# Kernel tuning notes

Measured on AMD Instinct MI355X. Metric: run time of the kernel, lower is better.

Reference implementation:

```python
import jax, jax.numpy as jnp
import numpy as np

IN_DIM = 4096
OUT_DIM = 4096
RANK = 16
BATCH = 4
SEQ = 2048


def setup_inputs() -> dict:
    key = jax.random.key(0)
    ks = jax.random.split(key, 7)
    x = jax.random.normal(ks[0], (BATCH, SEQ, IN_DIM), dtype=jnp.float32)
    org_weight = jax.random.normal(ks[1], (OUT_DIM, IN_DIM), dtype=jnp.float32) * 0.02
    org_bias = jax.random.normal(ks[2], (OUT_DIM,), dtype=jnp.float32) * 0.02
    hada_w1_a = jax.random.normal(ks[3], (OUT_DIM, RANK), dtype=jnp.float32) * 0.1
    hada_w1_b = jax.random.normal(ks[4], (RANK, IN_DIM), dtype=jnp.float32)
    hada_w2_a = jax.random.normal(ks[5], (OUT_DIM, RANK), dtype=jnp.float32) * 0.1
    hada_w2_b = jax.random.normal(ks[6], (RANK, IN_DIM), dtype=jnp.float32)
    scalar = jnp.ones((), dtype=jnp.float32)
    return {
        "x": x,
        "org_weight": org_weight,
        "org_bias": org_bias,
        "hada_w1_a": hada_w1_a,
        "hada_w1_b": hada_w1_b,
        "hada_w2_a": hada_w2_a,
        "hada_w2_b": hada_w2_b,
        "scalar": scalar,
    }


def reference(x, org_weight, org_bias, hada_w1_a, hada_w1_b, hada_w2_a, hada_w2_b, scalar):
    scale = jnp.asarray(1.0, dtype=hada_w1_b.dtype)   # self.scale = 1.0
    multiplier = jnp.asarray(1.0, dtype=x.dtype)       # self.multiplier = 1.0
    # base = F.linear(x, org_weight, org_bias)
    base = jnp.einsum("bsi,oi->bso", x, org_weight) + org_bias
    # diff_weight = (w1a @ w1b) * (w2a @ w2b) * scale * scalar  -> [out, in]
    diff_weight = (hada_w1_a @ hada_w1_b) * (hada_w2_a @ hada_w2_b) * scale * scalar
    # delta = F.linear(x, diff_weight * multiplier)
    delta = jnp.einsum("bsi,oi->bso", x, diff_weight * multiplier)
    return base + delta
```

## Files before the change

kernel.cpp:

```cpp
#include <hip/hip_runtime.h>

#define IN_DIM 4096
#define OUT_DIM 4096
#define RANK 16
#define MDIM 8192

typedef unsigned short ushort_t;
typedef __attribute__((ext_vector_type(8))) short short8;
typedef __attribute__((ext_vector_type(4))) float floatx4;
typedef __attribute__((ext_vector_type(4))) ushort_t ushort4_t;
typedef __attribute__((ext_vector_type(2))) ushort_t ushort2_t;

__device__ __forceinline__ ushort_t f2b(float f) {
    union { float f; unsigned int i; } v; v.f = f;
    unsigned int u = v.i;
    u += 0x7FFFu + ((u >> 16) & 1u);
    return (ushort_t)(u >> 16);
}

#define GLOAD_LDS16(gp, lp)                                                    \
    __builtin_amdgcn_global_load_lds(                                          \
        (__attribute__((address_space(1))) void*)(gp),                         \
        (__attribute__((address_space(3))) void*)(lp), 16, 0, 0)

__global__ __launch_bounds__(256) void convx_kernel(
    const float4* __restrict__ x, ushort4_t* __restrict__ xb, int n4)
{
    int i = blockIdx.x * blockDim.x + threadIdx.x;
    int stride = gridDim.x * blockDim.x;
    for (; i < n4; i += stride) {
        float4 v = x[i];
        ushort4_t o;
        o.x = f2b(v.x); o.y = f2b(v.y); o.z = f2b(v.z); o.w = f2b(v.w);
        xb[i] = o;
    }
}

__global__ __launch_bounds__(256) void weff_kernel(
    const float* __restrict__ orgw,
    const float* __restrict__ w1a, const float* __restrict__ w1b,
    const float* __restrict__ w2a, const float* __restrict__ w2b,
    const float* __restrict__ scalar,
    ushort_t* __restrict__ weff)
{
    __shared__ float s1a[64 * RANK];
    __shared__ float s2a[64 * RANK];

    const int t  = threadIdx.x;
    const int i0 = blockIdx.x * 512 + t * 2;
    const int o0 = blockIdx.y * 64;

    for (int e = t; e < 64 * RANK; e += 256) {
        s1a[e] = w1a[o0 * RANK + e];
        s2a[e] = w2a[o0 * RANK + e];
    }

    float b1[RANK][2], b2[RANK][2];
    #pragma unroll
    for (int r = 0; r < RANK; ++r) {
        const float2 v1 = *(const float2*)&w1b[r * IN_DIM + i0];
        const float2 v2 = *(const float2*)&w2b[r * IN_DIM + i0];
        b1[r][0] = v1.x; b1[r][1] = v1.y;
        b2[r][0] = v2.x; b2[r][1] = v2.y;
    }
    __syncthreads();

    const float sc = scalar[0];
    for (int o = 0; o < 64; ++o) {
        float4 a1v[4], a2v[4];
        #pragma unroll
        for (int j = 0; j < 4; ++j) {
            a1v[j] = *(const float4*)&s1a[o * RANK + j * 4];
            a2v[j] = *(const float4*)&s2a[o * RANK + j * 4];
        }
        float p1_0 = 0.f, p1_1 = 0.f, p2_0 = 0.f, p2_1 = 0.f;
        #pragma unroll
        for (int j = 0; j < 4; ++j) {
            #pragma unroll
            for (int k = 0; k < 4; ++k) {
                const int r = j * 4 + k;
                const float a1 = (k == 0) ? a1v[j].x : (k == 1) ? a1v[j].y
                               : (k == 2) ? a1v[j].z : a1v[j].w;
                const float a2 = (k == 0) ? a2v[j].x : (k == 1) ? a2v[j].y
                               : (k == 2) ? a2v[j].z : a2v[j].w;
                p1_0 += a1 * b1[r][0]; p1_1 += a1 * b1[r][1];
                p2_0 += a2 * b2[r][0]; p2_1 += a2 * b2[r][1];
            }
        }
        const size_t idx = (size_t)(o0 + o) * IN_DIM + i0;
        const float2 ov = *(const float2*)&orgw[idx];
        ushort2_t st;
        st.x = f2b(ov.x + p1_0 * p2_0 * sc);
        st.y = f2b(ov.y + p1_1 * p2_1 * sc);
        *(ushort2_t*)&weff[idx] = st;
    }
}

#define BM 256
#define BN 256
#define BK 64

#define STAGE_A(buf, half, kcol)                                               \
    do {                                                                       \
        GLOAD_LDS16(gX0 + (size_t)(half) * (128 * IN_DIM) + (kcol),            \
                    (short*)&lA[buf][half][0][0] + w * 512);                   \
        GLOAD_LDS16(gX1 + (size_t)(half) * (128 * IN_DIM) + (kcol),            \
                    (short*)&lA[buf][half][0][0] + 4096 + w * 512);            \
    } while (0)

#define STAGE_B(buf, half, kcol)                                               \
    do {                                                                       \
        GLOAD_LDS16(gW0 + (size_t)(half) * (128 * IN_DIM) + (kcol),            \
                    (short*)&lB[buf][half][0][0] + w * 512);                   \
        GLOAD_LDS16(gW1 + (size_t)(half) * (128 * IN_DIM) + (kcol),            \
                    (short*)&lB[buf][half][0][0] + 4096 + w * 512);            \
    } while (0)

#define MFMA_(d, a, b) (d) = __builtin_amdgcn_mfma_f32_16x16x32_bf16((a), (b), (d), 0, 0, 0)

#define HALF_ITER(aB, bB, S1, S2, S3, S4)                                      \
    do {                                                                       \
        short8 a_lo[4][2], a_hi[4][2], b_lo[2][2], b_hi[2][2];                 \
        S1;                                                                    \
                           \
        _Pragma("unroll")                                                      \
        for (int mi = 0; mi < 4; ++mi) {                                       \
            a_lo[mi][0] = *(const short8*)((aB) + mi * 1024 + ok0);            \
            a_lo[mi][1] = *(const short8*)((aB) + mi * 1024 + ok1);            \
        }                                                                      \
        _Pragma("unroll")                                                      \
        for (int ni = 0; ni < 2; ++ni) {                                       \
            b_lo[ni][0] = *(const short8*)((bB) + ni * 1024 + ok0);            \
            b_lo[ni][1] = *(const short8*)((bB) + ni * 1024 + ok1);            \
        }                                                                      \
        asm volatile("" ::: "memory");                  \
                                     \
        _Pragma("unroll")                                                      \
        for (int mi = 0; mi < 4; ++mi) {                                       \
            a_hi[mi][0] = *(const short8*)((aB) + 4096 + mi * 1024 + ok0);     \
            a_hi[mi][1] = *(const short8*)((aB) + 4096 + mi * 1024 + ok1);     \
        }                                                                      \
        asm volatile("" ::: "memory");                  \
                                     \
        _Pragma("unroll")                                                      \
        for (int ni = 0; ni < 2; ++ni) {                                       \
            b_hi[ni][0] = *(const short8*)((bB) + 2048 + ni * 1024 + ok0);     \
            b_hi[ni][1] = *(const short8*)((bB) + 2048 + ni * 1024 + ok1);     \
        }                                                                      \
          \
        __builtin_amdgcn_s_barrier();                                          \
        asm volatile("s_waitcnt lgkmcnt(12)" ::: "memory");                    \
        __builtin_amdgcn_sched_barrier(0);                                     \
        __builtin_amdgcn_s_setprio(1);                                         \
        _Pragma("unroll")                                                      \
        for (int mi = 0; mi < 4; ++mi)                                         \
            _Pragma("unroll")                                                  \
            for (int ni = 0; ni < 2; ++ni) {                                   \
                MFMA_(acc[mi][ni], a_lo[mi][0], b_lo[ni][0]);                  \
                MFMA_(acc[mi][ni], a_lo[mi][1], b_lo[ni][1]);                  \
            }                                                                  \
        __builtin_amdgcn_s_setprio(0);                                         \
        __builtin_amdgcn_s_barrier();                                          \
                         \
        S2;                                                                    \
        __builtin_amdgcn_s_barrier();                                          \
        asm volatile("s_waitcnt lgkmcnt(4)" ::: "memory");                     \
        __builtin_amdgcn_sched_barrier(0);                                     \
        __builtin_amdgcn_s_setprio(1);                                         \
        _Pragma("unroll")                                                      \
        for (int mi = 0; mi < 4; ++mi)                                         \
            _Pragma("unroll")                                                  \
            for (int ni = 0; ni < 2; ++ni) {                                   \
                MFMA_(acc[4 + mi][ni], a_hi[mi][0], b_lo[ni][0]);              \
                MFMA_(acc[4 + mi][ni], a_hi[mi][1], b_lo[ni][1]);              \
            }                                                                  \
        __builtin_amdgcn_s_setprio(0);                                         \
        __builtin_amdgcn_s_barrier();                                          \
                                     \
        S3;                                                                    \
        __builtin_amdgcn_s_barrier();                                          \
        asm volatile("s_waitcnt lgkmcnt(0)" ::: "memory");                     \
        __builtin_amdgcn_sched_barrier(0);                                     \
        __builtin_amdgcn_s_setprio(1);                                         \
        _Pragma("unroll")                                                      \
        for (int mi = 0; mi < 4; ++mi)                                         \
            _Pragma("unroll")                                                  \
            for (int ni = 0; ni < 2; ++ni) {                                   \
                MFMA_(acc[4 + mi][2 + ni], a_hi[mi][0], b_hi[ni][0]);          \
                MFMA_(acc[4 + mi][2 + ni], a_hi[mi][1], b_hi[ni][1]);          \
            }                                                                  \
        __builtin_amdgcn_s_setprio(0);                                         \
        __builtin_amdgcn_s_barrier();                                          \
                  \
        S4;                                                                    \
        __builtin_amdgcn_s_barrier();                                          \
        __builtin_amdgcn_s_setprio(1);                                         \
        _Pragma("unroll")                                                      \
        for (int mi = 0; mi < 4; ++mi)                                         \
            _Pragma("unroll")                                                  \
            for (int ni = 0; ni < 2; ++ni) {                                   \
                MFMA_(acc[mi][2 + ni], a_lo[mi][0], b_hi[ni][0]);              \
                MFMA_(acc[mi][2 + ni], a_lo[mi][1], b_hi[ni][1]);              \
            }                                                                  \
        __builtin_amdgcn_s_setprio(0);                                         \
        asm volatile("s_waitcnt vmcnt(4)" ::: "memory");                       \
        __builtin_amdgcn_s_barrier();                                          \
    } while (0)

__global__ __launch_bounds__(512, 2) void gemm_kernel(
    const ushort_t* __restrict__ X,
    const ushort_t* __restrict__ W,
    const float* __restrict__ bias,
    float* __restrict__ out)
{
    __shared__ __align__(16) short lA[2][2][128][64];
    __shared__ __align__(16) short lB[2][2][128][64];

    const int t    = threadIdx.x;
    const int w    = t >> 6;
    const int lane = t & 63;
    const int quad = lane >> 4;
    const int r16  = lane & 15;
    const int wm   = w >> 2;
    const int wn   = w & 3;

    const int bid = blockIdx.y * gridDim.x + blockIdx.x;
    const int swz = (bid & 7) * 64 + (bid >> 3);
    const int m0  = (swz >> 4) * BM;
    const int n0  = (swz & 15) * BN;

    const int s0  = w * 64 + lane;
    const int s1  = 512 + s0;
    const int r0  = s0 >> 3, r1 = s1 >> 3;
    const int k80 = (s0 & 7) ^ (r0 & 7);
    const int k81 = (s1 & 7) ^ (r1 & 7);
    const ushort_t* gX0 = X + (size_t)(m0 + r0) * IN_DIM + k80 * 8;
    const ushort_t* gX1 = X + (size_t)(m0 + r1) * IN_DIM + k81 * 8;
    const ushort_t* gW0 = W + (size_t)(n0 + r0) * IN_DIM + k80 * 8;
    const ushort_t* gW1 = W + (size_t)(n0 + r1) * IN_DIM + k81 * 8;

    const short* aB0 = &lA[0][wm][r16][0];
    const short* aB1 = &lA[1][wm][r16][0];
    const short* bB0 = &lB[0][wn >> 1][(wn & 1) * 64 + r16][0];
    const short* bB1 = &lB[1][wn >> 1][(wn & 1) * 64 + r16][0];
    const int ok0 = ((0 + quad) ^ (r16 & 7)) << 3;
    const int ok1 = ((4 + quad) ^ (r16 & 7)) << 3;

    floatx4 acc[8][4];
    #pragma unroll
    for (int i = 0; i < 8; ++i)
        #pragma unroll
        for (int j = 0; j < 4; ++j)
            acc[i][j] = (floatx4){0.f, 0.f, 0.f, 0.f};

    STAGE_A(0, 0, 0);
    STAGE_A(0, 1, 0);
    STAGE_B(0, 0, 0);
    STAGE_B(0, 1, 0);
    STAGE_A(1, 0, 64);
    STAGE_A(1, 1, 64);
    asm volatile("s_waitcnt vmcnt(4)" ::: "memory");
    __builtin_amdgcn_s_barrier();

    for (int it = 0; it < IN_DIM / 128; ++it) {
        const int kmax = IN_DIM - 64;
        int kB1 = it * 128 + 64;  if (kB1 > kmax) kB1 = kmax;
        int kA2 = it * 128 + 128; if (kA2 > kmax) kA2 = kmax;
        int kA3 = it * 128 + 192; if (kA3 > kmax) kA3 = kmax;

        HALF_ITER(aB0, bB0,
                  STAGE_B(1, 0, kB1), STAGE_B(1, 1, kB1),
                  STAGE_A(0, 0, kA2), STAGE_A(0, 1, kA2));
        HALF_ITER(aB1, bB1,
                  STAGE_B(0, 0, kA2), STAGE_B(0, 1, kA2),
                  STAGE_A(1, 0, kA3), STAGE_A(1, 1, kA3));
    }

    #pragma unroll
    for (int ni = 0; ni < 4; ++ni) {
        const int gn = n0 + wn * 64 + ni * 16 + r16;
        const float bv = bias[gn];
        #pragma unroll
        for (int mi = 0; mi < 8; ++mi) {
            const int gm = m0 + wm * 128 + mi * 16 + quad * 4;
            #pragma unroll
            for (int rr = 0; rr < 4; ++rr)
                out[(size_t)(gm + rr) * OUT_DIM + gn] = acc[mi][ni][rr] + bv;
        }
    }
}

extern "C" void kernel_launch(void* const* d_in, const int* in_sizes, int n_in,
                              void* d_out, int out_size, void* d_ws, size_t ws_size,
                              hipStream_t stream) {
    const float* x      = (const float*)d_in[0];
    const float* orgw   = (const float*)d_in[1];
    const float* bias   = (const float*)d_in[2];
    const float* w1a    = (const float*)d_in[3];
    const float* w1b    = (const float*)d_in[4];
    const float* w2a    = (const float*)d_in[5];
    const float* w2b    = (const float*)d_in[6];
    const float* scalar = (const float*)d_in[7];

    ushort_t* xb   = (ushort_t*)d_ws;
    ushort_t* weff = (ushort_t*)d_ws + (size_t)MDIM * IN_DIM;
    float* out = (float*)d_out;

    const int n4 = MDIM * IN_DIM / 4;
    convx_kernel<<<2048, 256, 0, stream>>>((const float4*)x, (ushort4_t*)xb, n4);
    weff_kernel<<<dim3(IN_DIM / 512, OUT_DIM / 64), 256, 0, stream>>>(
        orgw, w1a, w1b, w2a, w2b, scalar, weff);
    gemm_kernel<<<dim3(OUT_DIM / BN, MDIM / BM), 512, 0, stream>>>(
        xb, weff, bias, out);
}
```

Baseline: 630.0 us.

## Merge x-conversion and weight-prep kernels and reorder GEMM LDS reads

Fuses the bf16 conversion of x and the effective-weight construction into one prep kernel, using a block-index split, so one launch replaces two and the two jobs can overlap. The weight loop is unrolled by 2 and loads the original weight before the rank-16 products. In the GEMM half-iteration, the LDS reads of the a_hi and b_hi fragments now sit between the MFMA phases instead of all being issued up front, and the waits become full lgkmcnt(0) waits without sched_barriers. This lowers register pressure and interleaves LDS traffic with staging, but it may expose more LDS latency.

Measured after the change: 556.7 us. -11.6%, faster.

```diff
diff --git a/kernel.cpp b/kernel.cpp
--- a/kernel.cpp
+++ b/kernel.cpp
@@ -23,20 +23,8 @@
         (__attribute__((address_space(1))) void*)(gp),                         \
         (__attribute__((address_space(3))) void*)(lp), 16, 0, 0)
 
-__global__ __launch_bounds__(256) void convx_kernel(
-    const float4* __restrict__ x, ushort4_t* __restrict__ xb, int n4)
-{
-    int i = blockIdx.x * blockDim.x + threadIdx.x;
-    int stride = gridDim.x * blockDim.x;
-    for (; i < n4; i += stride) {
-        float4 v = x[i];
-        ushort4_t o;
-        o.x = f2b(v.x); o.y = f2b(v.y); o.z = f2b(v.z); o.w = f2b(v.w);
-        xb[i] = o;
-    }
-}
-
-__global__ __launch_bounds__(256) void weff_kernel(
+__global__ __launch_bounds__(256) void prep_kernel(
+    const float4* __restrict__ x, ushort4_t* __restrict__ xb, int n4,
     const float* __restrict__ orgw,
     const float* __restrict__ w1a, const float* __restrict__ w1b,
     const float* __restrict__ w2a, const float* __restrict__ w2b,
@@ -46,53 +34,68 @@
     __shared__ float s1a[64 * RANK];
     __shared__ float s2a[64 * RANK];
 
-    const int t  = threadIdx.x;
-    const int i0 = blockIdx.x * 512 + t * 2;
-    const int o0 = blockIdx.y * 64;
-
-    for (int e = t; e < 64 * RANK; e += 256) {
-        s1a[e] = w1a[o0 * RANK + e];
-        s2a[e] = w2a[o0 * RANK + e];
-    }
-
-    float b1[RANK][2], b2[RANK][2];
-    #pragma unroll
-    for (int r = 0; r < RANK; ++r) {
-        const float2 v1 = *(const float2*)&w1b[r * IN_DIM + i0];
-        const float2 v2 = *(const float2*)&w2b[r * IN_DIM + i0];
-        b1[r][0] = v1.x; b1[r][1] = v1.y;
-        b2[r][0] = v2.x; b2[r][1] = v2.y;
-    }
-    __syncthreads();
-
-    const float sc = scalar[0];
-    for (int o = 0; o < 64; ++o) {
-        float4 a1v[4], a2v[4];
+    const int bid = blockIdx.x;
+    const int t   = threadIdx.x;
+
+    if (bid < 512) {
+        const int i0 = (bid & 7) * 512 + t * 2;
+        const int o0 = (bid >> 3) * 64;
+
+        for (int e = t; e < 64 * RANK; e += 256) {
+            s1a[e] = w1a[o0 * RANK + e];
+            s2a[e] = w2a[o0 * RANK + e];
+        }
+
+        float b1[RANK][2], b2[RANK][2];
         #pragma unroll
-        for (int j = 0; j < 4; ++j) {
-            a1v[j] = *(const float4*)&s1a[o * RANK + j * 4];
-            a2v[j] = *(const float4*)&s2a[o * RANK + j * 4];
-        }
-        float p1_0 = 0.f, p1_1 = 0.f, p2_0 = 0.f, p2_1 = 0.f;
-        #pragma unroll
-        for (int j = 0; j < 4; ++j) {
+        for (int r = 0; r < RANK; ++r) {
+            const float2 v1 = *(const float2*)&w1b[r * IN_DIM + i0];
+            const float2 v2 = *(const float2*)&w2b[r * IN_DIM + i0];
+            b1[r][0] = v1.x; b1[r][1] = v1.y;
+            b2[r][0] = v2.x; b2[r][1] = v2.y;
+        }
+        __syncthreads();
+
+        const float sc = scalar[0];
+        #pragma unroll 2
+        for (int o = 0; o < 64; ++o) {
+            const size_t idx = (size_t)(o0 + o) * IN_DIM + i0;
+            const float2 ov = *(const float2*)&orgw[idx];
+            float4 a1v[4], a2v[4];
             #pragma unroll
-            for (int k = 0; k < 4; ++k) {
-                const int r = j * 4 + k;
-                const float a1 = (k == 0) ? a1v[j].x : (k == 1) ? a1v[j].y
-                               : (k == 2) ? a1v[j].z : a1v[j].w;
-                const float a2 = (k == 0) ? a2v[j].x : (k == 1) ? a2v[j].y
-                               : (k == 2) ? a2v[j].z : a2v[j].w;
-                p1_0 += a1 * b1[r][0]; p1_1 += a1 * b1[r][1];
-                p2_0 += a2 * b2[r][0]; p2_1 += a2 * b2[r][1];
+            for (int j = 0; j < 4; ++j) {
+                a1v[j] = *(const float4*)&s1a[o * RANK + j * 4];
+                a2v[j] = *(const float4*)&s2a[o * RANK + j * 4];
             }
-        }
-        const size_t idx = (size_t)(o0 + o) * IN_DIM + i0;
-        const float2 ov = *(const float2*)&orgw[idx];
-        ushort2_t st;
-        st.x = f2b(ov.x + p1_0 * p2_0 * sc);
-        st.y = f2b(ov.y + p1_1 * p2_1 * sc);
-        *(ushort2_t*)&weff[idx] = st;
+            float p1_0 = 0.f, p1_1 = 0.f, p2_0 = 0.f, p2_1 = 0.f;
+            #pragma unroll
+            for (int j = 0; j < 4; ++j) {
+                #pragma unroll
+                for (int k = 0; k < 4; ++k) {
+                    const int r = j * 4 + k;
+                    const float a1 = (k == 0) ? a1v[j].x : (k == 1) ? a1v[j].y
+                                   : (k == 2) ? a1v[j].z : a1v[j].w;
+                    const float a2 = (k == 0) ? a2v[j].x : (k == 1) ? a2v[j].y
+                                   : (k == 2) ? a2v[j].z : a2v[j].w;
+                    p1_0 += a1 * b1[r][0]; p1_1 += a1 * b1[r][1];
+                    p2_0 += a2 * b2[r][0]; p2_1 += a2 * b2[r][1];
+                }
+            }
+            ushort2_t st;
+            st.x = f2b(ov.x + p1_0 * p2_0 * sc);
+            st.y = f2b(ov.y + p1_1 * p2_1 * sc);
+            *(ushort2_t*)&weff[idx] = st;
+        }
+    } else {
+        const int nblk = 2048;
+        int i = (bid - 512) * 256 + t;
+        const int stride = nblk * 256;
+        for (; i < n4; i += stride) {
+            float4 v = x[i];
+            ushort4_t o;
+            o.x = f2b(v.x); o.y = f2b(v.y); o.z = f2b(v.z); o.w = f2b(v.w);
+            xb[i] = o;
+        }
     }
 }
 
@@ -121,8 +124,7 @@
 #define HALF_ITER(aB, bB, S1, S2, S3, S4)                                      \
     do {                                                                       \
         short8 a_lo[4][2], a_hi[4][2], b_lo[2][2], b_hi[2][2];                 \
-        S1;                                                                    \
-                           \
+                         \
         _Pragma("unroll")                                                      \
         for (int mi = 0; mi < 4; ++mi) {                                       \
             a_lo[mi][0] = *(const short8*)((aB) + mi * 1024 + ok0);            \
@@ -133,24 +135,9 @@
             b_lo[ni][0] = *(const short8*)((bB) + ni * 1024 + ok0);            \
             b_lo[ni][1] = *(const short8*)((bB) + ni * 1024 + ok1);            \
         }                                                                      \
-        asm volatile("" ::: "memory");                  \
-                                     \
-        _Pragma("unroll")                                                      \
-        for (int mi = 0; mi < 4; ++mi) {                                       \
-            a_hi[mi][0] = *(const short8*)((aB) + 4096 + mi * 1024 + ok0);     \
-            a_hi[mi][1] = *(const short8*)((aB) + 4096 + mi * 1024 + ok1);     \
-        }                                                                      \
-        asm volatile("" ::: "memory");                  \
-                                     \
-        _Pragma("unroll")                                                      \
-        for (int ni = 0; ni < 2; ++ni) {                                       \
-            b_hi[ni][0] = *(const short8*)((bB) + 2048 + ni * 1024 + ok0);     \
-            b_hi[ni][1] = *(const short8*)((bB) + 2048 + ni * 1024 + ok1);     \
-        }                                                                      \
-          \
-        __builtin_amdgcn_s_barrier();                                          \
-        asm volatile("s_waitcnt lgkmcnt(12)" ::: "memory");                    \
-        __builtin_amdgcn_sched_barrier(0);                                     \
+        S1;                                                                    \
+        __builtin_amdgcn_s_barrier();                                          \
+        asm volatile("s_waitcnt lgkmcnt(0)" ::: "memory");                     \
         __builtin_amdgcn_s_setprio(1);                                         \
         _Pragma("unroll")                                                      \
         for (int mi = 0; mi < 4; ++mi)                                         \
@@ -161,11 +148,15 @@
             }                                                                  \
         __builtin_amdgcn_s_setprio(0);                                         \
         __builtin_amdgcn_s_barrier();                                          \
-                         \
+                                 \
+        _Pragma("unroll")                                                      \
+        for (int mi = 0; mi < 4; ++mi) {                                       \
+            a_hi[mi][0] = *(const short8*)((aB) + 4096 + mi * 1024 + ok0);     \
+            a_hi[mi][1] = *(const short8*)((aB) + 4096 + mi * 1024 + ok1);     \
+        }                                                                      \
         S2;                                                                    \
         __builtin_amdgcn_s_barrier();                                          \
-        asm volatile("s_waitcnt lgkmcnt(4)" ::: "memory");                     \
-        __builtin_amdgcn_sched_barrier(0);                                     \
+        asm volatile("s_waitcnt lgkmcnt(0)" ::: "memory");                     \
         __builtin_amdgcn_s_setprio(1);                                         \
         _Pragma("unroll")                                                      \
         for (int mi = 0; mi < 4; ++mi)                                         \
@@ -176,11 +167,15 @@
             }                                                                  \
         __builtin_amdgcn_s_setprio(0);                                         \
         __builtin_amdgcn_s_barrier();                                          \
-                                     \
+                                 \
+        _Pragma("unroll")                                                      \
+        for (int ni = 0; ni < 2; ++ni) {                                       \
+            b_hi[ni][0] = *(const short8*)((bB) + 2048 + ni * 1024 + ok0);     \
+            b_hi[ni][1] = *(const short8*)((bB) + 2048 + ni * 1024 + ok1);     \
+        }                                                                      \
         S3;                                                                    \
         __builtin_amdgcn_s_barrier();                                          \
         asm volatile("s_waitcnt lgkmcnt(0)" ::: "memory");                     \
-        __builtin_amdgcn_sched_barrier(0);                                     \
         __builtin_amdgcn_s_setprio(1);                                         \
         _Pragma("unroll")                                                      \
         for (int mi = 0; mi < 4; ++mi)                                         \
@@ -191,7 +186,7 @@
             }                                                                  \
         __builtin_amdgcn_s_setprio(0);                                         \
         __builtin_amdgcn_s_barrier();                                          \
-                  \
+           \
         S4;                                                                    \
         __builtin_amdgcn_s_barrier();                                          \
         __builtin_amdgcn_s_setprio(1);                                         \
@@ -307,8 +302,8 @@
     float* out = (float*)d_out;
 
     const int n4 = MDIM * IN_DIM / 4;
-    convx_kernel<<<2048, 256, 0, stream>>>((const float4*)x, (ushort4_t*)xb, n4);
-    weff_kernel<<<dim3(IN_DIM / 512, OUT_DIM / 64), 256, 0, stream>>>(
+    prep_kernel<<<2560, 256, 0, stream>>>(
+        (const float4*)x, (ushort4_t*)xb, n4,
         orgw, w1a, w1b, w2a, w2b, scalar, weff);
     gemm_kernel<<<dim3(OUT_DIM / BN, MDIM / BM), 512, 0, stream>>>(
         xb, weff, bias, out);
```
